# Performance work log

Measured on AMD Instinct MI355X. Metric: run time of the kernel, lower is better.

Reference implementation:

```python
import jax, jax.numpy as jnp
from jax import lax
import numpy as np

WIN = 9
PAD = WIN // 2
DN = ('NCDHW', 'OIDHW', 'NCDHW')


def box_sum(x):
    """9x9x9 all-ones box sum (same padding), computed separably per axis.
    Matches the original dense depthwise conv3d with a ones kernel exactly in math."""
    C = x.shape[1]
    for axis in range(3):  # spatial axes D, H, W
        kshape = [1, 1, 1]
        kshape[axis] = WIN
        kernel = jnp.ones((C, 1, *kshape), dtype=x.dtype)
        padding = [(PAD, PAD) if i == axis else (0, 0) for i in range(3)]
        x = lax.conv_general_dilated(
            x, kernel, window_strides=(1, 1, 1), padding=padding,
            dimension_numbers=DN, feature_group_count=C)
    return x


def setup_inputs() -> dict:
    key = jax.random.key(0)
    k1, k2 = jax.random.split(key)
    shape = (2, 1, 160, 192, 160)
    y_true = jax.random.uniform(k1, shape, dtype=jnp.float32)
    y_pred = jax.random.uniform(k2, shape, dtype=jnp.float32)
    return {"y_true": y_true, "y_pred": y_pred}


def reference(y_true, y_pred):
    Ii, Ji = y_true, y_pred
    win_size = jnp.asarray(WIN ** 3, dtype=Ii.dtype)

    I_sum = box_sum(Ii)
    J_sum = box_sum(Ji)
    I2_sum = box_sum(Ii * Ii)
    J2_sum = box_sum(Ji * Ji)
    IJ_sum = box_sum(Ii * Ji)

    u_I = I_sum / win_size
    u_J = J_sum / win_size

    cross = IJ_sum - u_I * J_sum
    I_var = jnp.maximum(I2_sum - u_I * I_sum, 1e-05)
    J_var = jnp.maximum(J2_sum - u_J * J_sum, 1e-05)

    cc = cross * cross / (I_var * J_var + 1e-05)
    return -jnp.sum(cc)
```

## Files before the change

kernel.cpp:

```cpp
#include <hip/hip_runtime.h>
#include <hip/hip_fp16.h>

#define ND 2
#define DD 160
#define HH 192
#define WW 160
#define HW (HH * WW)
#define DHW (DD * HH * WW)
#define VOX (ND * DHW)

__device__ __forceinline__ void slide4(const float x[12], float S[4]) {
    float f = ((x[0] + x[1]) + (x[2] + x[3]))
            + ((x[4] + x[5]) + (x[6] + x[7])) + x[8];
    S[0] = f;
    f += x[9]  - x[0]; S[1] = f;
    f += x[10] - x[1]; S[2] = f;
    f += x[11] - x[2]; S[3] = f;
}

constexpr int P1TW  = 32;
constexpr int P1TH  = 16;
constexpr int P1HLO = P1TH + 8;

__global__ __launch_bounds__(256)
void ncc_pass1(const float* __restrict__ I, const float* __restrict__ J,
               __half* __restrict__ ws)
{
    __shared__ float4 sws[P1HLO][P1TW + 1];
    __shared__ float  sw4[P1HLO][P1TW + 1];

    const int tid = threadIdx.x;
    const int w0  = blockIdx.x * P1TW;
    const int h0  = blockIdx.y * P1TH;
    const int z   = blockIdx.z;
    const int sbase = z * HW;

    if (tid < 192) {
        const int arow = tid >> 3;
        const int ag   = tid & 7;
        const int agh  = h0 + arow - 4;
        const bool ahok = (agh >= 0) && (agh < HH);
        const int rbase = sbase + agh * WW;
        const int agws  = w0 + ag * 4 - 4;

        float a[12], b[12];
        #pragma unroll
        for (int c = 0; c < 3; ++c) {
            const int gw = agws + 4 * c;
            float4 va = make_float4(0.f, 0.f, 0.f, 0.f), vb = va;
            if (ahok && gw >= 0 && gw < WW) {
                va = *(const float4*)(I + rbase + gw);
                vb = *(const float4*)(J + rbase + gw);
                va.x -= 0.5f; va.y -= 0.5f; va.z -= 0.5f; va.w -= 0.5f;
                vb.x -= 0.5f; vb.y -= 0.5f; vb.z -= 0.5f; vb.w -= 0.5f;
            }
            *(float4*)&a[4 * c] = va;
            *(float4*)&b[4 * c] = vb;
        }
        float S0[4], S1[4], S2[4], S3[4], S4[4], f[12];
        slide4(a, S0);
        slide4(b, S1);
        #pragma unroll
        for (int i = 0; i < 12; ++i) f[i] = a[i] * a[i];
        slide4(f, S2);
        #pragma unroll
        for (int i = 0; i < 12; ++i) f[i] = b[i] * b[i];
        slide4(f, S3);
        #pragma unroll
        for (int i = 0; i < 12; ++i) f[i] = a[i] * b[i];
        slide4(f, S4);
        #pragma unroll
        for (int t = 0; t < 4; ++t) {
            sws[arow][ag * 4 + t] = make_float4(S0[t], S1[t], S2[t], S3[t]);
            sw4[arow][ag * 4 + t] = S4[t];
        }
    }
    __syncthreads();

    const int oh2 = tid >> 5;
    const int h   = oh2 * 2;
    const int ow  = tid & 31;
    float t0 = 0.f, t1 = 0.f, t2 = 0.f, t3 = 0.f, t4 = 0.f;
    float f0x, f0y, f0z, f0w, f04;
    {
        const float4 v = sws[h][ow];
        f0x = v.x; f0y = v.y; f0z = v.z; f0w = v.w;
        f04 = sw4[h][ow];
        t0 = v.x; t1 = v.y; t2 = v.z; t3 = v.w; t4 = f04;
    }
    #pragma unroll
    for (int q = 1; q < 9; ++q) {
        const float4 v = sws[h + q][ow];
        t0 += v.x; t1 += v.y; t2 += v.z; t3 += v.w;
        t4 += sw4[h + q][ow];
    }
    float u0, u1, u2, u3, u4;
    {
        const float4 v = sws[h + 9][ow];
        u0 = t0 + v.x - f0x;
        u1 = t1 + v.y - f0y;
        u2 = t2 + v.z - f0z;
        u3 = t3 + v.w - f0w;
        u4 = t4 + sw4[h + 9][ow] - f04;
    }
    const int g = sbase + (h0 + h) * WW + (w0 + ow);
    ws[0 * VOX + g] = __float2half(t0);
    ws[1 * VOX + g] = __float2half(t1);
    ws[2 * VOX + g] = __float2half(t2);
    ws[3 * VOX + g] = __float2half(t3);
    ws[4 * VOX + g] = __float2half(t4);
    ws[0 * VOX + g + WW] = __float2half(u0);
    ws[1 * VOX + g + WW] = __float2half(u1);
    ws[2 * VOX + g + WW] = __float2half(u2);
    ws[3 * VOX + g + WW] = __float2half(u3);
    ws[4 * VOX + g + WW] = __float2half(u4);
}

constexpr int P2CH = 40;
constexpr int P2NS = P2CH + 8;

__global__ __launch_bounds__(256)
void ncc_pass2(const __half* __restrict__ ws, float* __restrict__ outp)
{
    const int col = blockIdx.x * 256 + threadIdx.x;
    const int d0  = blockIdx.y * P2CH;
    const int n   = col / HW;
    const int rem = col - n * HW;
    const int h   = rem / WW;
    const int w   = rem - h * WW;
    const int base = n * DHW + rem;

    const float cW = (float)(min(w + 4, WW - 1) - max(w - 4, 0) + 1);
    const float cH = (float)(min(h + 4, HH - 1) - max(h - 4, 0) + 1);
    const float cHW = cW * cH;

    float ring[5][9];
    #pragma unroll
    for (int p = 0; p < 5; ++p)
        #pragma unroll
        for (int q = 0; q < 9; ++q) ring[p][q] = 0.f;
    float run0 = 0.f, run1 = 0.f, run2 = 0.f, run3 = 0.f, run4 = 0.f;
    float acc = 0.f;
    const float inv = 1.0f / 729.0f;

    #pragma unroll 1
    for (int g = 0; g < 6; ++g) {
        #pragma unroll
        for (int jj = 0; jj < 9; ++jj) {
            const int s = g * 9 + jj;
            if (s < P2NS) {
                const int dd = d0 - 4 + s;
                float v0 = 0.f, v1 = 0.f, v2 = 0.f, v3 = 0.f, v4 = 0.f;
                if (dd >= 0 && dd < DD) {
                    const int a = base + dd * HW;
                    v0 = __half2float(ws[0 * VOX + a]);
                    v1 = __half2float(ws[1 * VOX + a]);
                    v2 = __half2float(ws[2 * VOX + a]);
                    v3 = __half2float(ws[3 * VOX + a]);
                    v4 = __half2float(ws[4 * VOX + a]);
                }
                run0 += v0 - ring[0][jj]; ring[0][jj] = v0;
                run1 += v1 - ring[1][jj]; ring[1][jj] = v1;
                run2 += v2 - ring[2][jj]; ring[2][jj] = v2;
                run3 += v3 - ring[3][jj]; ring[3][jj] = v3;
                run4 += v4 - ring[4][jj]; ring[4][jj] = v4;

                if (s >= 8) {
                    const int d = d0 + s - 8;
                    const float cD  = (float)(min(d + 4, DD - 1) - max(d - 4, 0) + 1);
                    const float cnt = cHW * cD;
                    const float Is  = run0 + 0.5f * cnt;
                    const float Js  = run1 + 0.5f * cnt;
                    const float I2  = run2 + run0 + 0.25f * cnt;
                    const float J2  = run3 + run1 + 0.25f * cnt;
                    const float IJ  = run4 + 0.5f * (run0 + run1) + 0.25f * cnt;
                    const float uI = Is * inv, uJ = Js * inv;
                    const float cross = IJ - uI * Js;
                    const float Iv = fmaxf(I2 - uI * Is, 1e-5f);
                    const float Jv = fmaxf(J2 - uJ * Js, 1e-5f);
                    acc += cross * cross / (Iv * Jv + 1e-5f);
                }
            }
        }
    }

    __shared__ float wred[4];
    #pragma unroll
    for (int off = 32; off > 0; off >>= 1)
        acc += __shfl_down(acc, off, 64);
    const int lane = threadIdx.x & 63, wid = threadIdx.x >> 6;
    if (lane == 0) wred[wid] = acc;
    __syncthreads();
    if (threadIdx.x == 0)
        atomicAdd(outp, -(wred[0] + wred[1] + wred[2] + wred[3]));
}

constexpr int FTW = 16, FTH = 16, FHLO = FTH + 8;
constexpr int FCH = 20, FNCH = DD / FCH, FNSL = FCH + 8, FNR = FNSL / 2;

__global__ __launch_bounds__(256, 4)
void ncc_fused(const float* __restrict__ I, const float* __restrict__ J,
               float* __restrict__ outp)
{
    __shared__ float4 sws[2][FHLO][FTW + 1];
    __shared__ float  sw4[2][FHLO][FTW + 1];
    __shared__ float  wred[4];

    const int tid = threadIdx.x;
    const int w0 = blockIdx.x * FTW, h0 = blockIdx.y * FTH;
    const int z = blockIdx.z, n = z / FNCH, d0 = (z % FNCH) * FCH;
    const int lane = tid & 63, wid = tid >> 6;
    const int oh = tid >> 4, ow = tid & 15;
    const bool ajob = (tid < 192);
    const int sl = tid / 96, rj = tid - sl * 96;
    const int arow = rj >> 2, awg = rj & 3;
    const int agh = h0 + arow - 4, agws = w0 + awg * 4 - 4;
    const bool ahok = (agh >= 0) && (agh < HH);

    float rbuf[5][9];
    #pragma unroll
    for (int p = 0; p < 5; ++p)
        #pragma unroll
        for (int q = 0; q < 9; ++q) rbuf[p][q] = 0.f;
    float run0 = 0.f, run1 = 0.f, run2 = 0.f, run3 = 0.f, run4 = 0.f;
    float acc = 0.f;
    const float inv = 1.0f / 729.0f;

    #pragma unroll 1
    for (int g = 0; g < 2; ++g) {
        #pragma unroll
        for (int r = 0; r < 9; ++r) {
            const int rr = g * 9 + r;
            if (rr < FNR) {
                const int s0 = 2 * rr, dd0 = d0 - 4 + s0;
                if (ajob) {
                    const int dd = dd0 + sl;
                    if (dd >= 0 && dd < DD) {
                        float a[12], b[12];
                        const int rbase = (n * DD + dd) * HW + agh * WW;
                        #pragma unroll
                        for (int c = 0; c < 3; ++c) {
                            const int gw = agws + 4 * c;
                            float4 va = make_float4(0.f, 0.f, 0.f, 0.f), vb = va;
                            if (ahok && gw >= 0 && gw < WW) {
                                va = *(const float4*)(I + rbase + gw);
                                vb = *(const float4*)(J + rbase + gw);
                            }
                            *(float4*)&a[4 * c] = va;
                            *(float4*)&b[4 * c] = vb;
                        }
                        float S0[4], S1[4], S2[4], S3[4], S4[4], f[12];
                        slide4(a, S0);
                        slide4(b, S1);
                        #pragma unroll
                        for (int i = 0; i < 12; ++i) f[i] = a[i] * a[i];
                        slide4(f, S2);
                        #pragma unroll
                        for (int i = 0; i < 12; ++i) f[i] = b[i] * b[i];
                        slide4(f, S3);
                        #pragma unroll
                        for (int i = 0; i < 12; ++i) f[i] = a[i] * b[i];
                        slide4(f, S4);
                        #pragma unroll
                        for (int t = 0; t < 4; ++t) {
                            sws[sl][arow][awg * 4 + t] =
                                make_float4(S0[t], S1[t], S2[t], S3[t]);
                            sw4[sl][arow][awg * 4 + t] = S4[t];
                        }
                    }
                }
                __syncthreads();
                #pragma unroll
                for (int half = 0; half < 2; ++half) {
                    const int ddx = dd0 + half, sx = s0 + half;
                    float t0 = 0.f, t1 = 0.f, t2 = 0.f, t3 = 0.f, t4 = 0.f;
                    if (ddx >= 0 && ddx < DD) {
                        #pragma unroll
                        for (int q = 0; q < 9; ++q) {
                            const float4 v = sws[half][oh + q][ow];
                            t0 += v.x; t1 += v.y; t2 += v.z; t3 += v.w;
                            t4 += sw4[half][oh + q][ow];
                        }
                    }
                    const int jj = (2 * r + half) % 9;
                    run0 += t0 - rbuf[0][jj]; rbuf[0][jj] = t0;
                    run1 += t1 - rbuf[1][jj]; rbuf[1][jj] = t1;
                    run2 += t2 - rbuf[2][jj]; rbuf[2][jj] = t2;
                    run3 += t3 - rbuf[3][jj]; rbuf[3][jj] = t3;
                    run4 += t4 - rbuf[4][jj]; rbuf[4][jj] = t4;
                    if (sx >= 8) {
                        const float uI = run0 * inv, uJ = run1 * inv;
                        const float cross = run4 - uI * run1;
                        const float Iv = fmaxf(run2 - uI * run0, 1e-5f);
                        const float Jv = fmaxf(run3 - uJ * run1, 1e-5f);
                        acc += cross * cross / (Iv * Jv + 1e-5f);
                    }
                }
                __syncthreads();
            }
        }
    }
    #pragma unroll
    for (int off = 32; off > 0; off >>= 1)
        acc += __shfl_down(acc, off, 64);
    if (lane == 0) wred[wid] = acc;
    __syncthreads();
    if (tid == 0)
        atomicAdd(outp, -(wred[0] + wred[1] + wred[2] + wred[3]));
}

extern "C" void kernel_launch(void* const* d_in, const int* in_sizes, int n_in,
                              void* d_out, int out_size, void* d_ws, size_t ws_size,
                              hipStream_t stream)
{
    const float* I = (const float*)d_in[0];
    const float* J = (const float*)d_in[1];
    float* out = (float*)d_out;

    hipMemsetAsync(out, 0, sizeof(float), stream);

    const size_t need = (size_t)5 * VOX * sizeof(__half);
    if (ws_size >= need) {
        __half* ws = (__half*)d_ws;
        dim3 g1(WW / P1TW, HH / P1TH, ND * DD);
        ncc_pass1<<<g1, 256, 0, stream>>>(I, J, ws);
        dim3 g2(ND * HW / 256, DD / P2CH);
        ncc_pass2<<<g2, 256, 0, stream>>>(ws, out);
    } else {
        dim3 grid(WW / FTW, HH / FTH, ND * FNCH);
        ncc_fused<<<grid, 256, 0, stream>>>(I, J, out);
    }
}
```

Baseline: 189.5 us.

## Interleave fp16 workspace channels, enlarge pass1 tile, halve pass2 depth chunk, drop memset

The workspace is now interleaved as two half2 arrays (channels 0/1 and 2/3) plus one half array, so pass2 issues three loads per voxel instead of five. Pass1 tiles grow to 24 rows, with all 256 threads doing the W pass and each output thread producing three rows, which cuts halo overhead. Pass2's depth chunk shrinks from 40 to 20 to raise parallelism, at the cost of more re-read halo. The output memset is replaced by a zero write from the first pass1 block, which relies on stream ordering ahead of pass2's atomics.

```diff
diff --git a/kernel.cpp b/kernel.cpp
--- a/kernel.cpp
+++ b/kernel.cpp
@@ -19,12 +19,13 @@
 }
 
 constexpr int P1TW  = 32;
-constexpr int P1TH  = 16;
+constexpr int P1TH  = 24;
 constexpr int P1HLO = P1TH + 8;
 
 __global__ __launch_bounds__(256)
 void ncc_pass1(const float* __restrict__ I, const float* __restrict__ J,
-               __half* __restrict__ ws)
+               __half2* __restrict__ ws01, __half2* __restrict__ ws23,
+               __half* __restrict__ ws4, float* __restrict__ outp)
 {
     __shared__ float4 sws[P1HLO][P1TW + 1];
     __shared__ float  sw4[P1HLO][P1TW + 1];
@@ -35,7 +36,10 @@
     const int z   = blockIdx.z;
     const int sbase = z * HW;
 
-    if (tid < 192) {
+    if (tid == 0 && blockIdx.x == 0 && blockIdx.y == 0 && blockIdx.z == 0)
+        *outp = 0.f;
+
+    {
         const int arow = tid >> 3;
         const int ag   = tid & 7;
         const int agh  = h0 + arow - 4;
@@ -77,19 +81,26 @@
     }
     __syncthreads();
 
-    const int oh2 = tid >> 5;
-    const int h   = oh2 * 2;
+    const int oh3 = tid >> 5;
+    const int h   = oh3 * 3;
     const int ow  = tid & 31;
-    float t0 = 0.f, t1 = 0.f, t2 = 0.f, t3 = 0.f, t4 = 0.f;
-    float f0x, f0y, f0z, f0w, f04;
+    float t0, t1, t2, t3, t4;
+    float r0x, r0y, r0z, r0w, r04;
+    float r1x, r1y, r1z, r1w, r14;
     {
         const float4 v = sws[h][ow];
-        f0x = v.x; f0y = v.y; f0z = v.z; f0w = v.w;
-        f04 = sw4[h][ow];
-        t0 = v.x; t1 = v.y; t2 = v.z; t3 = v.w; t4 = f04;
-    }
-    #pragma unroll
-    for (int q = 1; q < 9; ++q) {
+        r0x = v.x; r0y = v.y; r0z = v.z; r0w = v.w;
+        r04 = sw4[h][ow];
+        t0 = r0x; t1 = r0y; t2 = r0z; t3 = r0w; t4 = r04;
+    }
+    {
+        const float4 v = sws[h + 1][ow];
+        r1x = v.x; r1y = v.y; r1z = v.z; r1w = v.w;
+        r14 = sw4[h + 1][ow];
+        t0 += r1x; t1 += r1y; t2 += r1z; t3 += r1w; t4 += r14;
+    }
+    #pragma unroll
+    for (int q = 2; q < 9; ++q) {
         const float4 v = sws[h + q][ow];
         t0 += v.x; t1 += v.y; t2 += v.z; t3 += v.w;
         t4 += sw4[h + q][ow];
@@ -97,30 +108,40 @@
     float u0, u1, u2, u3, u4;
     {
         const float4 v = sws[h + 9][ow];
-        u0 = t0 + v.x - f0x;
-        u1 = t1 + v.y - f0y;
-        u2 = t2 + v.z - f0z;
-        u3 = t3 + v.w - f0w;
-        u4 = t4 + sw4[h + 9][ow] - f04;
+        u0 = t0 + v.x - r0x;
+        u1 = t1 + v.y - r0y;
+        u2 = t2 + v.z - r0z;
+        u3 = t3 + v.w - r0w;
+        u4 = t4 + sw4[h + 9][ow] - r04;
+    }
+    float v0, v1, v2, v3, v4;
+    {
+        const float4 v = sws[h + 10][ow];
+        v0 = u0 + v.x - r1x;
+        v1 = u1 + v.y - r1y;
+        v2 = u2 + v.z - r1z;
+        v3 = u3 + v.w - r1w;
+        v4 = u4 + sw4[h + 10][ow] - r14;
     }
     const int g = sbase + (h0 + h) * WW + (w0 + ow);
-    ws[0 * VOX + g] = __float2half(t0);
-    ws[1 * VOX + g] = __float2half(t1);
-    ws[2 * VOX + g] = __float2half(t2);
-    ws[3 * VOX + g] = __float2half(t3);
-    ws[4 * VOX + g] = __float2half(t4);
-    ws[0 * VOX + g + WW] = __float2half(u0);
-    ws[1 * VOX + g + WW] = __float2half(u1);
-    ws[2 * VOX + g + WW] = __float2half(u2);
-    ws[3 * VOX + g + WW] = __float2half(u3);
-    ws[4 * VOX + g + WW] = __float2half(u4);
-}
-
-constexpr int P2CH = 40;
+    __half2 p;
+    p.x = __float2half(t0); p.y = __float2half(t1); ws01[g] = p;
+    p.x = __float2half(t2); p.y = __float2half(t3); ws23[g] = p;
+    ws4[g] = __float2half(t4);
+    p.x = __float2half(u0); p.y = __float2half(u1); ws01[g + WW] = p;
+    p.x = __float2half(u2); p.y = __float2half(u3); ws23[g + WW] = p;
+    ws4[g + WW] = __float2half(u4);
+    p.x = __float2half(v0); p.y = __float2half(v1); ws01[g + 2 * WW] = p;
+    p.x = __float2half(v2); p.y = __float2half(v3); ws23[g + 2 * WW] = p;
+    ws4[g + 2 * WW] = __float2half(v4);
+}
+
+constexpr int P2CH = 20;
 constexpr int P2NS = P2CH + 8;
 
 __global__ __launch_bounds__(256)
-void ncc_pass2(const __half* __restrict__ ws, float* __restrict__ outp)
+void ncc_pass2(const __half2* __restrict__ ws01, const __half2* __restrict__ ws23,
+               const __half* __restrict__ ws4, float* __restrict__ outp)
 {
     const int col = blockIdx.x * 256 + threadIdx.x;
     const int d0  = blockIdx.y * P2CH;
@@ -144,7 +165,7 @@
     const float inv = 1.0f / 729.0f;
 
     #pragma unroll 1
-    for (int g = 0; g < 6; ++g) {
+    for (int g = 0; g < 4; ++g) {
         #pragma unroll
         for (int jj = 0; jj < 9; ++jj) {
             const int s = g * 9 + jj;
@@ -153,11 +174,13 @@
                 float v0 = 0.f, v1 = 0.f, v2 = 0.f, v3 = 0.f, v4 = 0.f;
                 if (dd >= 0 && dd < DD) {
                     const int a = base + dd * HW;
-                    v0 = __half2float(ws[0 * VOX + a]);
-                    v1 = __half2float(ws[1 * VOX + a]);
-                    v2 = __half2float(ws[2 * VOX + a]);
-                    v3 = __half2float(ws[3 * VOX + a]);
-                    v4 = __half2float(ws[4 * VOX + a]);
+                    const __half2 x01 = ws01[a];
+                    const __half2 x23 = ws23[a];
+                    v0 = __half2float(x01.x);
+                    v1 = __half2float(x01.y);
+                    v2 = __half2float(x23.x);
+                    v3 = __half2float(x23.y);
+                    v4 = __half2float(ws4[a]);
                 }
                 run0 += v0 - ring[0][jj]; ring[0][jj] = v0;
                 run1 += v1 - ring[1][jj]; ring[1][jj] = v1;
@@ -317,16 +340,17 @@
     const float* J = (const float*)d_in[1];
     float* out = (float*)d_out;
 
-    hipMemsetAsync(out, 0, sizeof(float), stream);
-
-    const size_t need = (size_t)5 * VOX * sizeof(__half);
+    const size_t need = (size_t)10 * VOX;
     if (ws_size >= need) {
-        __half* ws = (__half*)d_ws;
+        __half2* ws01 = (__half2*)d_ws;
+        __half2* ws23 = ws01 + (size_t)VOX;
+        __half*  ws4  = (__half*)(ws01 + 2 * (size_t)VOX);
         dim3 g1(WW / P1TW, HH / P1TH, ND * DD);
-        ncc_pass1<<<g1, 256, 0, stream>>>(I, J, ws);
+        ncc_pass1<<<g1, 256, 0, stream>>>(I, J, ws01, ws23, ws4, out);
         dim3 g2(ND * HW / 256, DD / P2CH);
-        ncc_pass2<<<g2, 256, 0, stream>>>(ws, out);
+        ncc_pass2<<<g2, 256, 0, stream>>>(ws01, ws23, ws4, out);
     } else {
+        hipMemsetAsync(out, 0, sizeof(float), stream);
         dim3 grid(WW / FTW, HH / FTH, ND * FNCH);
         ncc_fused<<<grid, 256, 0, stream>>>(I, J, out);
     }
```

Result: slower. 193.3 us (+2.0%).

## Interleave four half workspace channels, enlarge H tile, fold output zeroing into pass1

Applied to the files above, without the earlier changes.

The workspace now stores the first four box-sum channels interleaved as one 8-byte half4 record per voxel, plus a separate half plane for the fifth. Pass2 therefore issues one 8-byte load and one 2-byte load per voxel instead of five scattered 2-byte loads, and pass1 writes with the same wider stores. Pass1 tiles are doubled in H to 32 rows, so each thread emits four output rows and the 8-row halo is amortised over more work. The separate memset is replaced by pass1 block 0 zeroing the output, which removes one stream operation but relies on kernel ordering on the stream.

```diff
diff --git a/kernel.cpp b/kernel.cpp
--- a/kernel.cpp
+++ b/kernel.cpp
@@ -9,6 +9,8 @@
 #define DHW (DD * HH * WW)
 #define VOX (ND * DHW)
 
+struct alignas(8) h4 { __half2 lo, hi; };
+
 __device__ __forceinline__ void slide4(const float x[12], float S[4]) {
     float f = ((x[0] + x[1]) + (x[2] + x[3]))
             + ((x[4] + x[5]) + (x[6] + x[7])) + x[8];
@@ -19,12 +21,13 @@
 }
 
 constexpr int P1TW  = 32;
-constexpr int P1TH  = 16;
+constexpr int P1TH  = 32;
 constexpr int P1HLO = P1TH + 8;
 
 __global__ __launch_bounds__(256)
 void ncc_pass1(const float* __restrict__ I, const float* __restrict__ J,
-               __half* __restrict__ ws)
+               h4* __restrict__ ws0123, __half* __restrict__ ws4,
+               float* __restrict__ outp)
 {
     __shared__ float4 sws[P1HLO][P1TW + 1];
     __shared__ float  sw4[P1HLO][P1TW + 1];
@@ -35,9 +38,12 @@
     const int z   = blockIdx.z;
     const int sbase = z * HW;
 
-    if (tid < 192) {
-        const int arow = tid >> 3;
-        const int ag   = tid & 7;
+    if (tid == 0 && blockIdx.x == 0 && blockIdx.y == 0 && blockIdx.z == 0)
+        *outp = 0.f;
+
+    for (int job = tid; job < 8 * P1HLO; job += 256) {
+        const int arow = job >> 3;
+        const int ag   = job & 7;
         const int agh  = h0 + arow - 4;
         const bool ahok = (agh >= 0) && (agh < HH);
         const int rbase = sbase + agh * WW;
@@ -77,19 +83,29 @@
     }
     __syncthreads();
 
-    const int oh2 = tid >> 5;
-    const int h   = oh2 * 2;
-    const int ow  = tid & 31;
-    float t0 = 0.f, t1 = 0.f, t2 = 0.f, t3 = 0.f, t4 = 0.f;
-    float f0x, f0y, f0z, f0w, f04;
+    const int h  = (tid >> 5) * 4;
+    const int ow = tid & 31;
+    float t0, t1, t2, t3, t4;
+    float a0x, a0y, a0z, a0w, a04;
+    float a1x, a1y, a1z, a1w, a14;
+    float a2x, a2y, a2z, a2w, a24;
     {
         const float4 v = sws[h][ow];
-        f0x = v.x; f0y = v.y; f0z = v.z; f0w = v.w;
-        f04 = sw4[h][ow];
-        t0 = v.x; t1 = v.y; t2 = v.z; t3 = v.w; t4 = f04;
-    }
-    #pragma unroll
-    for (int q = 1; q < 9; ++q) {
+        a0x = v.x; a0y = v.y; a0z = v.z; a0w = v.w; a04 = sw4[h][ow];
+        t0 = a0x; t1 = a0y; t2 = a0z; t3 = a0w; t4 = a04;
+    }
+    {
+        const float4 v = sws[h + 1][ow];
+        a1x = v.x; a1y = v.y; a1z = v.z; a1w = v.w; a14 = sw4[h + 1][ow];
+        t0 += a1x; t1 += a1y; t2 += a1z; t3 += a1w; t4 += a14;
+    }
+    {
+        const float4 v = sws[h + 2][ow];
+        a2x = v.x; a2y = v.y; a2z = v.z; a2w = v.w; a24 = sw4[h + 2][ow];
+        t0 += a2x; t1 += a2y; t2 += a2z; t3 += a2w; t4 += a24;
+    }
+    #pragma unroll
+    for (int q = 3; q < 9; ++q) {
         const float4 v = sws[h + q][ow];
         t0 += v.x; t1 += v.y; t2 += v.z; t3 += v.w;
         t4 += sw4[h + q][ow];
@@ -97,30 +113,48 @@
     float u0, u1, u2, u3, u4;
     {
         const float4 v = sws[h + 9][ow];
-        u0 = t0 + v.x - f0x;
-        u1 = t1 + v.y - f0y;
-        u2 = t2 + v.z - f0z;
-        u3 = t3 + v.w - f0w;
-        u4 = t4 + sw4[h + 9][ow] - f04;
+        u0 = t0 + v.x - a0x;
+        u1 = t1 + v.y - a0y;
+        u2 = t2 + v.z - a0z;
+        u3 = t3 + v.w - a0w;
+        u4 = t4 + sw4[h + 9][ow] - a04;
+    }
+    float v0, v1, v2, v3, v4;
+    {
+        const float4 v = sws[h + 10][ow];
+        v0 = u0 + v.x - a1x;
+        v1 = u1 + v.y - a1y;
+        v2 = u2 + v.z - a1z;
+        v3 = u3 + v.w - a1w;
+        v4 = u4 + sw4[h + 10][ow] - a14;
+    }
+    float x0, x1, x2, x3, x4;
+    {
+        const float4 v = sws[h + 11][ow];
+        x0 = v0 + v.x - a2x;
+        x1 = v1 + v.y - a2y;
+        x2 = v2 + v.z - a2z;
+        x3 = v3 + v.w - a2w;
+        x4 = v4 + sw4[h + 11][ow] - a24;
     }
     const int g = sbase + (h0 + h) * WW + (w0 + ow);
-    ws[0 * VOX + g] = __float2half(t0);
-    ws[1 * VOX + g] = __float2half(t1);
-    ws[2 * VOX + g] = __float2half(t2);
-    ws[3 * VOX + g] = __float2half(t3);
-    ws[4 * VOX + g] = __float2half(t4);
-    ws[0 * VOX + g + WW] = __float2half(u0);
-    ws[1 * VOX + g + WW] = __float2half(u1);
-    ws[2 * VOX + g + WW] = __float2half(u2);
-    ws[3 * VOX + g + WW] = __float2half(u3);
-    ws[4 * VOX + g + WW] = __float2half(u4);
+    h4 p;
+    p.lo = __floats2half2_rn(t0, t1); p.hi = __floats2half2_rn(t2, t3);
+    ws0123[g] = p;             ws4[g] = __float2half(t4);
+    p.lo = __floats2half2_rn(u0, u1); p.hi = __floats2half2_rn(u2, u3);
+    ws0123[g + WW] = p;        ws4[g + WW] = __float2half(u4);
+    p.lo = __floats2half2_rn(v0, v1); p.hi = __floats2half2_rn(v2, v3);
+    ws0123[g + 2 * WW] = p;    ws4[g + 2 * WW] = __float2half(v4);
+    p.lo = __floats2half2_rn(x0, x1); p.hi = __floats2half2_rn(x2, x3);
+    ws0123[g + 3 * WW] = p;    ws4[g + 3 * WW] = __float2half(x4);
 }
 
 constexpr int P2CH = 40;
 constexpr int P2NS = P2CH + 8;
 
 __global__ __launch_bounds__(256)
-void ncc_pass2(const __half* __restrict__ ws, float* __restrict__ outp)
+void ncc_pass2(const h4* __restrict__ ws0123, const __half* __restrict__ ws4,
+               float* __restrict__ outp)
 {
     const int col = blockIdx.x * 256 + threadIdx.x;
     const int d0  = blockIdx.y * P2CH;
@@ -153,11 +187,12 @@
                 float v0 = 0.f, v1 = 0.f, v2 = 0.f, v3 = 0.f, v4 = 0.f;
                 if (dd >= 0 && dd < DD) {
                     const int a = base + dd * HW;
-                    v0 = __half2float(ws[0 * VOX + a]);
-                    v1 = __half2float(ws[1 * VOX + a]);
-                    v2 = __half2float(ws[2 * VOX + a]);
-                    v3 = __half2float(ws[3 * VOX + a]);
-                    v4 = __half2float(ws[4 * VOX + a]);
+                    const h4 q = ws0123[a];
+                    v0 = __half2float(q.lo.x);
+                    v1 = __half2float(q.lo.y);
+                    v2 = __half2float(q.hi.x);
+                    v3 = __half2float(q.hi.y);
+                    v4 = __half2float(ws4[a]);
                 }
                 run0 += v0 - ring[0][jj]; ring[0][jj] = v0;
                 run1 += v1 - ring[1][jj]; ring[1][jj] = v1;
@@ -317,16 +352,16 @@
     const float* J = (const float*)d_in[1];
     float* out = (float*)d_out;
 
-    hipMemsetAsync(out, 0, sizeof(float), stream);
-
-    const size_t need = (size_t)5 * VOX * sizeof(__half);
+    const size_t need = (size_t)10 * VOX;
     if (ws_size >= need) {
-        __half* ws = (__half*)d_ws;
+        h4* ws0123 = (h4*)d_ws;
+        __half* ws4 = (__half*)(ws0123 + (size_t)VOX);
         dim3 g1(WW / P1TW, HH / P1TH, ND * DD);
-        ncc_pass1<<<g1, 256, 0, stream>>>(I, J, ws);
+        ncc_pass1<<<g1, 256, 0, stream>>>(I, J, ws0123, ws4, out);
         dim3 g2(ND * HW / 256, DD / P2CH);
-        ncc_pass2<<<g2, 256, 0, stream>>>(ws, out);
+        ncc_pass2<<<g2, 256, 0, stream>>>(ws0123, ws4, out);
     } else {
+        hipMemsetAsync(out, 0, sizeof(float), stream);
         dim3 grid(WW / FTW, HH / FTH, ND * FNCH);
         ncc_fused<<<grid, 256, 0, stream>>>(I, J, out);
     }
```

Result: faster. 180.5 us (-4.8%).

## Replace two-pass workspace pipeline with single fused kernel using shared-memory fp16 ring

Applied to the files above, without the earlier changes.

Drops the two-kernel path that wrote the five separable H/W partial sums to a global fp16 workspace and re-read them for the depth pass. A single 512-thread fused kernel now does the W and H box sums in shared memory per depth-slice pair and keeps the 9-deep depth ring buffer in shared memory as fp16, which saves registers. Inputs are centered by 0.5 and border counts are corrected exactly as in the old pass2, so fp16 rounding behaves the same. This removes the workspace round trip to HBM. In exchange each block recomputes an 8-slice depth halo per 40-slice chunk, synchronises twice per slice pair, and uses a larger shared-memory footprint that may limit occupancy.

```diff
diff --git a/kernel.cpp b/kernel.cpp
--- a/kernel.cpp
+++ b/kernel.cpp
@@ -7,7 +7,16 @@
 #define WW 160
 #define HW (HH * WW)
 #define DHW (DD * HH * WW)
-#define VOX (ND * DHW)
+
+constexpr int TW  = 32;
+constexpr int TH  = 16;
+constexpr int HLO = TH + 8;
+constexpr int FCH = 40;
+constexpr int NCH = DD / FCH;
+constexpr int NSL = FCH + 8;
+constexpr int NR  = NSL / 2;
+
+struct alignas(8) h4 { __half2 lo, hi; };
 
 __device__ __forceinline__ void slide4(const float x[12], float S[4]) {
     float f = ((x[0] + x[1]) + (x[2] + x[3]))
@@ -18,226 +27,63 @@
     f += x[11] - x[2]; S[3] = f;
 }
 
-constexpr int P1TW  = 32;
-constexpr int P1TH  = 16;
-constexpr int P1HLO = P1TH + 8;
-
-__global__ __launch_bounds__(256)
-void ncc_pass1(const float* __restrict__ I, const float* __restrict__ J,
-               __half* __restrict__ ws)
+__global__ __launch_bounds__(512, 4)
+void ncc_fused2(const float* __restrict__ I, const float* __restrict__ J,
+                float* __restrict__ outp)
 {
-    __shared__ float4 sws[P1HLO][P1TW + 1];
-    __shared__ float  sw4[P1HLO][P1TW + 1];
+    __shared__ float4 sws[2][HLO][TW + 1];
+    __shared__ float  sw4[2][HLO][TW + 1];
+    __shared__ h4     ring4[9][512];
+    __shared__ __half ring1[9][512];
+    __shared__ float  wred[8];
 
     const int tid = threadIdx.x;
-    const int w0  = blockIdx.x * P1TW;
-    const int h0  = blockIdx.y * P1TH;
+    const int w0  = blockIdx.x * TW;
+    const int h0  = blockIdx.y * TH;
     const int z   = blockIdx.z;
-    const int sbase = z * HW;
+    const int n   = z >> 2;
+    const int d0  = (z & 3) * FCH;
 
-    if (tid < 192) {
-        const int arow = tid >> 3;
-        const int ag   = tid & 7;
-        const int agh  = h0 + arow - 4;
-        const bool ahok = (agh >= 0) && (agh < HH);
-        const int rbase = sbase + agh * WW;
-        const int agws  = w0 + ag * 4 - 4;
+    const bool ajob = (tid < 384);
+    const int  sl   = tid / 192;
+    const int  rj   = tid - sl * 192;
+    const int  arow = rj >> 3;
+    const int  awg  = rj & 7;
+    const int  agh  = h0 + arow - 4;
+    const bool ahok = (agh >= 0) && (agh < HH);
+    const int  agws = w0 + awg * 4 - 4;
 
-        float a[12], b[12];
-        #pragma unroll
-        for (int c = 0; c < 3; ++c) {
-            const int gw = agws + 4 * c;
-            float4 va = make_float4(0.f, 0.f, 0.f, 0.f), vb = va;
-            if (ahok && gw >= 0 && gw < WW) {
-                va = *(const float4*)(I + rbase + gw);
-                vb = *(const float4*)(J + rbase + gw);
-                va.x -= 0.5f; va.y -= 0.5f; va.z -= 0.5f; va.w -= 0.5f;
-                vb.x -= 0.5f; vb.y -= 0.5f; vb.z -= 0.5f; vb.w -= 0.5f;
-            }
-            *(float4*)&a[4 * c] = va;
-            *(float4*)&b[4 * c] = vb;
-        }
-        float S0[4], S1[4], S2[4], S3[4], S4[4], f[12];
-        slide4(a, S0);
-        slide4(b, S1);
-        #pragma unroll
-        for (int i = 0; i < 12; ++i) f[i] = a[i] * a[i];
-        slide4(f, S2);
-        #pragma unroll
-        for (int i = 0; i < 12; ++i) f[i] = b[i] * b[i];
-        slide4(f, S3);
-        #pragma unroll
-        for (int i = 0; i < 12; ++i) f[i] = a[i] * b[i];
-        slide4(f, S4);
-        #pragma unroll
-        for (int t = 0; t < 4; ++t) {
-            sws[arow][ag * 4 + t] = make_float4(S0[t], S1[t], S2[t], S3[t]);
-            sw4[arow][ag * 4 + t] = S4[t];
-        }
-    }
-    __syncthreads();
-
-    const int oh2 = tid >> 5;
-    const int h   = oh2 * 2;
-    const int ow  = tid & 31;
-    float t0 = 0.f, t1 = 0.f, t2 = 0.f, t3 = 0.f, t4 = 0.f;
-    float f0x, f0y, f0z, f0w, f04;
-    {
-        const float4 v = sws[h][ow];
-        f0x = v.x; f0y = v.y; f0z = v.z; f0w = v.w;
-        f04 = sw4[h][ow];
-        t0 = v.x; t1 = v.y; t2 = v.z; t3 = v.w; t4 = f04;
-    }
-    #pragma unroll
-    for (int q = 1; q < 9; ++q) {
-        const float4 v = sws[h + q][ow];
-        t0 += v.x; t1 += v.y; t2 += v.z; t3 += v.w;
-        t4 += sw4[h + q][ow];
-    }
-    float u0, u1, u2, u3, u4;
-    {
-        const float4 v = sws[h + 9][ow];
-        u0 = t0 + v.x - f0x;
-        u1 = t1 + v.y - f0y;
-        u2 = t2 + v.z - f0z;
-        u3 = t3 + v.w - f0w;
-        u4 = t4 + sw4[h + 9][ow] - f04;
-    }
-    const int g = sbase + (h0 + h) * WW + (w0 + ow);
-    ws[0 * VOX + g] = __float2half(t0);
-    ws[1 * VOX + g] = __float2half(t1);
-    ws[2 * VOX + g] = __float2half(t2);
-    ws[3 * VOX + g] = __float2half(t3);
-    ws[4 * VOX + g] = __float2half(t4);
-    ws[0 * VOX + g + WW] = __float2half(u0);
-    ws[1 * VOX + g + WW] = __float2half(u1);
-    ws[2 * VOX + g + WW] = __float2half(u2);
-    ws[3 * VOX + g + WW] = __float2half(u3);
-    ws[4 * VOX + g + WW] = __float2half(u4);
-}
-
-constexpr int P2CH = 40;
-constexpr int P2NS = P2CH + 8;
-
-__global__ __launch_bounds__(256)
-void ncc_pass2(const __half* __restrict__ ws, float* __restrict__ outp)
-{
-    const int col = blockIdx.x * 256 + threadIdx.x;
-    const int d0  = blockIdx.y * P2CH;
-    const int n   = col / HW;
-    const int rem = col - n * HW;
-    const int h   = rem / WW;
-    const int w   = rem - h * WW;
-    const int base = n * DHW + rem;
-
-    const float cW = (float)(min(w + 4, WW - 1) - max(w - 4, 0) + 1);
-    const float cH = (float)(min(h + 4, HH - 1) - max(h - 4, 0) + 1);
+    const int oh = tid >> 5;
+    const int ow = tid & 31;
+    const int h  = h0 + oh, w = w0 + ow;
+    const float cW  = (float)(min(w + 4, WW - 1) - max(w - 4, 0) + 1);
+    const float cH  = (float)(min(h + 4, HH - 1) - max(h - 4, 0) + 1);
     const float cHW = cW * cH;
 
-    float ring[5][9];
-    #pragma unroll
-    for (int p = 0; p < 5; ++p)
+    {
+        h4 zz; zz.lo = __floats2half2_rn(0.f, 0.f); zz.hi = zz.lo;
+        const __half z1 = __float2half(0.f);
         #pragma unroll
-        for (int q = 0; q < 9; ++q) ring[p][q] = 0.f;
+        for (int q = 0; q < 9; ++q) { ring4[q][tid] = zz; ring1[q][tid] = z1; }
+    }
+
     float run0 = 0.f, run1 = 0.f, run2 = 0.f, run3 = 0.f, run4 = 0.f;
     float acc = 0.f;
     const float inv = 1.0f / 729.0f;
 
     #pragma unroll 1
-    for (int g = 0; g < 6; ++g) {
-        #pragma unroll
-        for (int jj = 0; jj < 9; ++jj) {
-            const int s = g * 9 + jj;
-            if (s < P2NS) {
-                const int dd = d0 - 4 + s;
-                float v0 = 0.f, v1 = 0.f, v2 = 0.f, v3 = 0.f, v4 = 0.f;
-                if (dd >= 0 && dd < DD) {
-                    const int a = base + dd * HW;
-                    v0 = __half2float(ws[0 * VOX + a]);
-                    v1 = __half2float(ws[1 * VOX + a]);
-                    v2 = __half2float(ws[2 * VOX + a]);
-                    v3 = __half2float(ws[3 * VOX + a]);
-                    v4 = __half2float(ws[4 * VOX + a]);
-                }
-                run0 += v0 - ring[0][jj]; ring[0][jj] = v0;
-                run1 += v1 - ring[1][jj]; ring[1][jj] = v1;
-                run2 += v2 - ring[2][jj]; ring[2][jj] = v2;
-                run3 += v3 - ring[3][jj]; ring[3][jj] = v3;
-                run4 += v4 - ring[4][jj]; ring[4][jj] = v4;
-
-                if (s >= 8) {
-                    const int d = d0 + s - 8;
-                    const float cD  = (float)(min(d + 4, DD - 1) - max(d - 4, 0) + 1);
-                    const float cnt = cHW * cD;
-                    const float Is  = run0 + 0.5f * cnt;
-                    const float Js  = run1 + 0.5f * cnt;
-                    const float I2  = run2 + run0 + 0.25f * cnt;
-                    const float J2  = run3 + run1 + 0.25f * cnt;
-                    const float IJ  = run4 + 0.5f * (run0 + run1) + 0.25f * cnt;
-                    const float uI = Is * inv, uJ = Js * inv;
-                    const float cross = IJ - uI * Js;
-                    const float Iv = fmaxf(I2 - uI * Is, 1e-5f);
-                    const float Jv = fmaxf(J2 - uJ * Js, 1e-5f);
-                    acc += cross * cross / (Iv * Jv + 1e-5f);
-                }
-            }
-        }
-    }
-
-    __shared__ float wred[4];
-    #pragma unroll
-    for (int off = 32; off > 0; off >>= 1)
-        acc += __shfl_down(acc, off, 64);
-    const int lane = threadIdx.x & 63, wid = threadIdx.x >> 6;
-    if (lane == 0) wred[wid] = acc;
-    __syncthreads();
-    if (threadIdx.x == 0)
-        atomicAdd(outp, -(wred[0] + wred[1] + wred[2] + wred[3]));
-}
-
-constexpr int FTW = 16, FTH = 16, FHLO = FTH + 8;
-constexpr int FCH = 20, FNCH = DD / FCH, FNSL = FCH + 8, FNR = FNSL / 2;
-
-__global__ __launch_bounds__(256, 4)
-void ncc_fused(const float* __restrict__ I, const float* __restrict__ J,
-               float* __restrict__ outp)
-{
-    __shared__ float4 sws[2][FHLO][FTW + 1];
-    __shared__ float  sw4[2][FHLO][FTW + 1];
-    __shared__ float  wred[4];
-
-    const int tid = threadIdx.x;
-    const int w0 = blockIdx.x * FTW, h0 = blockIdx.y * FTH;
-    const int z = blockIdx.z, n = z / FNCH, d0 = (z % FNCH) * FCH;
-    const int lane = tid & 63, wid = tid >> 6;
-    const int oh = tid >> 4, ow = tid & 15;
-    const bool ajob = (tid < 192);
-    const int sl = tid / 96, rj = tid - sl * 96;
-    const int arow = rj >> 2, awg = rj & 3;
-    const int agh = h0 + arow - 4, agws = w0 + awg * 4 - 4;
-    const bool ahok = (agh >= 0) && (agh < HH);
-
-    float rbuf[5][9];
-    #pragma unroll
-    for (int p = 0; p < 5; ++p)
-        #pragma unroll
-        for (int q = 0; q < 9; ++q) rbuf[p][q] = 0.f;
-    float run0 = 0.f, run1 = 0.f, run2 = 0.f, run3 = 0.f, run4 = 0.f;
-    float acc = 0.f;
-    const float inv = 1.0f / 729.0f;
-
-    #pragma unroll 1
-    for (int g = 0; g < 2; ++g) {
+    for (int g = 0; g < 3; ++g) {
         #pragma unroll
         for (int r = 0; r < 9; ++r) {
             const int rr = g * 9 + r;
-            if (rr < FNR) {
-                const int s0 = 2 * rr, dd0 = d0 - 4 + s0;
+            if (rr < NR) {
+                const int s0  = 2 * rr;
+                const int dd0 = d0 - 4 + s0;
                 if (ajob) {
                     const int dd = dd0 + sl;
                     if (dd >= 0 && dd < DD) {
+                        const int rbase = (n * DD + dd) * HW + agh * WW;
                         float a[12], b[12];
-                        const int rbase = (n * DD + dd) * HW + agh * WW;
                         #pragma unroll
                         for (int c = 0; c < 3; ++c) {
                             const int gw = agws + 4 * c;
@@ -245,6 +91,8 @@
                             if (ahok && gw >= 0 && gw < WW) {
                                 va = *(const float4*)(I + rbase + gw);
                                 vb = *(const float4*)(J + rbase + gw);
+                                va.x -= 0.5f; va.y -= 0.5f; va.z -= 0.5f; va.w -= 0.5f;
+                                vb.x -= 0.5f; vb.y -= 0.5f; vb.z -= 0.5f; vb.w -= 0.5f;
                             }
                             *(float4*)&a[4 * c] = va;
                             *(float4*)&b[4 * c] = vb;
@@ -272,7 +120,8 @@
                 __syncthreads();
                 #pragma unroll
                 for (int half = 0; half < 2; ++half) {
-                    const int ddx = dd0 + half, sx = s0 + half;
+                    const int s   = s0 + half;
+                    const int ddx = dd0 + half;
                     float t0 = 0.f, t1 = 0.f, t2 = 0.f, t3 = 0.f, t4 = 0.f;
                     if (ddx >= 0 && ddx < DD) {
                         #pragma unroll
@@ -282,17 +131,33 @@
                             t4 += sw4[half][oh + q][ow];
                         }
                     }
+                    h4 nh;
+                    nh.lo = __floats2half2_rn(t0, t1);
+                    nh.hi = __floats2half2_rn(t2, t3);
+                    const __half n4 = __float2half(t4);
                     const int jj = (2 * r + half) % 9;
-                    run0 += t0 - rbuf[0][jj]; rbuf[0][jj] = t0;
-                    run1 += t1 - rbuf[1][jj]; rbuf[1][jj] = t1;
-                    run2 += t2 - rbuf[2][jj]; rbuf[2][jj] = t2;
-                    run3 += t3 - rbuf[3][jj]; rbuf[3][jj] = t3;
-                    run4 += t4 - rbuf[4][jj]; rbuf[4][jj] = t4;
-                    if (sx >= 8) {
-                        const float uI = run0 * inv, uJ = run1 * inv;
-                        const float cross = run4 - uI * run1;
-                        const float Iv = fmaxf(run2 - uI * run0, 1e-5f);
-                        const float Jv = fmaxf(run3 - uJ * run1, 1e-5f);
+                    const h4     po = ring4[jj][tid];
+                    const __half p4 = ring1[jj][tid];
+                    run0 += __half2float(nh.lo.x) - __half2float(po.lo.x);
+                    run1 += __half2float(nh.lo.y) - __half2float(po.lo.y);
+                    run2 += __half2float(nh.hi.x) - __half2float(po.hi.x);
+                    run3 += __half2float(nh.hi.y) - __half2float(po.hi.y);
+                    run4 += __half2float(n4)      - __half2float(p4);
+                    ring4[jj][tid] = nh;
+                    ring1[jj][tid] = n4;
+                    if (s >= 8) {
+                        const int d = d0 + s - 8;
+                        const float cD  = (float)(min(d + 4, DD - 1) - max(d - 4, 0) + 1);
+                        const float cnt = cHW * cD;
+                        const float Is = run0 + 0.5f * cnt;
+                        const float Js = run1 + 0.5f * cnt;
+                        const float I2 = run2 + run0 + 0.25f * cnt;
+                        const float J2 = run3 + run1 + 0.25f * cnt;
+                        const float IJ = run4 + 0.5f * (run0 + run1) + 0.25f * cnt;
+                        const float uI = Is * inv, uJ = Js * inv;
+                        const float cross = IJ - uI * Js;
+                        const float Iv = fmaxf(I2 - uI * Is, 1e-5f);
+                        const float Jv = fmaxf(J2 - uJ * Js, 1e-5f);
                         acc += cross * cross / (Iv * Jv + 1e-5f);
                     }
                 }
@@ -300,13 +165,19 @@
             }
         }
     }
+
     #pragma unroll
     for (int off = 32; off > 0; off >>= 1)
         acc += __shfl_down(acc, off, 64);
+    const int lane = tid & 63, wid = tid >> 6;
     if (lane == 0) wred[wid] = acc;
     __syncthreads();
-    if (tid == 0)
-        atomicAdd(outp, -(wred[0] + wred[1] + wred[2] + wred[3]));
+    if (tid == 0) {
+        float s = 0.f;
+        #pragma unroll
+        for (int i = 0; i < 8; ++i) s += wred[i];
+        atomicAdd(outp, -s);
+    }
 }
 
 extern "C" void kernel_launch(void* const* d_in, const int* in_sizes, int n_in,
@@ -318,16 +189,6 @@
     float* out = (float*)d_out;
 
     hipMemsetAsync(out, 0, sizeof(float), stream);
-
-    const size_t need = (size_t)5 * VOX * sizeof(__half);
-    if (ws_size >= need) {
-        __half* ws = (__half*)d_ws;
-        dim3 g1(WW / P1TW, HH / P1TH, ND * DD);
-        ncc_pass1<<<g1, 256, 0, stream>>>(I, J, ws);
-        dim3 g2(ND * HW / 256, DD / P2CH);
-        ncc_pass2<<<g2, 256, 0, stream>>>(ws, out);
-    } else {
-        dim3 grid(WW / FTW, HH / FTH, ND * FNCH);
-        ncc_fused<<<grid, 256, 0, stream>>>(I, J, out);
-    }
+    dim3 grid(WW / TW, HH / TH, ND * NCH);
+    ncc_fused2<<<grid, 512, 0, stream>>>(I, J, out);
 }
```

New measurement: 166.4 us. 12.2% less time.
